# Performance work log

Measured on AMD Instinct MI355X. Metric: run time of the kernel, lower is better.

The kernel has to match this reference:

```python
import jax, jax.numpy as jnp
import numpy as np

B, S, HID = 4, 2048, 1024
H, DH = 16, 64  # HID = H * DH
ADP, NTASKS = 64, 10
GATE_S = 100.0  # s (soft gate temperature), != smax=400 so no hard threshold


def setup_inputs() -> dict:
    key = jax.random.key(0)
    ks = jax.random.split(key, 13)
    sc = 0.02
    return {
        "hidden_states": jax.random.normal(ks[0], (B, S, HID), jnp.float32),
        "Wq": jax.random.normal(ks[1], (HID, HID), jnp.float32) * sc,
        "bq": jax.random.normal(ks[2], (HID,), jnp.float32) * sc,
        "Wk": jax.random.normal(ks[3], (HID, HID), jnp.float32) * sc,
        "bk": jax.random.normal(ks[4], (HID,), jnp.float32) * sc,
        "Wv": jax.random.normal(ks[5], (HID, HID), jnp.float32) * sc,
        "bv": jax.random.normal(ks[6], (HID,), jnp.float32) * sc,
        "fc1_w": jax.random.normal(ks[7], (HID, ADP), jnp.float32) * sc,
        "fc1_b": jax.random.normal(ks[8], (ADP,), jnp.float32) * sc,
        "fc2_w": jax.random.normal(ks[9], (ADP, HID), jnp.float32) * sc,
        "fc2_b": jax.random.normal(ks[10], (HID,), jnp.float32) * sc,
        "efc1": jax.random.normal(ks[11], (NTASKS, ADP), jnp.float32),
        "efc2": jax.random.normal(ks[12], (NTASKS, HID), jnp.float32),
        "t": 3,
    }


def reference(hidden_states, Wq, bq, Wk, bk, Wv, bv,
              fc1_w, fc1_b, fc2_w, fc2_b, efc1, efc2, t):
    x = hidden_states
    # --- parallel adapter with task gates (add_residual=False) ---
    gfc1 = jax.nn.sigmoid(GATE_S * efc1[t])  # [ADP]
    gfc2 = jax.nn.sigmoid(GATE_S * efc2[t])  # [HID]
    h = jax.nn.relu(x @ fc1_w + fc1_b) * gfc1          # [B,S,ADP]
    adapter_out = jax.nn.relu(h @ fc2_w + fc2_b) * gfc2  # [B,S,HID]
    # --- multi-head self-attention (absolute positions, no mask, eval dropout) ---
    def split_heads(y):  # [B,S,HID] -> [B,H,S,DH]
        return y.reshape(B, S, H, DH).transpose(0, 2, 1, 3)
    q = split_heads(x @ Wq + bq)
    k = split_heads(x @ Wk + bk)
    v = split_heads(x @ Wv + bv)
    scores = jnp.einsum("bhqd,bhkd->bhqk", q, k) / np.sqrt(DH).astype(jnp.float32)
    probs = jax.nn.softmax(scores, axis=-1)
    ctx = jnp.einsum("bhqk,bhkd->bhqd", probs, v)
    ctx = ctx.transpose(0, 2, 1, 3).reshape(B, S, HID)
    return ctx + adapter_out
```

## Files before the change

kernel.cpp:

```cpp
#include <hip/hip_runtime.h>
#include <stdint.h>
#include <stddef.h>

typedef unsigned short u16;
typedef unsigned int u32;
typedef __bf16 bf16x8 __attribute__((ext_vector_type(8)));
typedef __bf16 bf16x4 __attribute__((ext_vector_type(4)));
typedef short s16x4 __attribute__((ext_vector_type(4)));
typedef float f32x4 __attribute__((ext_vector_type(4)));

#define BB  4
#define SS  2048
#define HIDD 1024
#define NH  16
#define DHD 64

#define GLD16(gaddr, laddr) \
  __builtin_amdgcn_global_load_lds( \
      (const __attribute__((address_space(1))) u32*)(gaddr), \
      (__attribute__((address_space(3))) u32*)(laddr), 16, 0, 0)

#define LDS_BARRIER() asm volatile("s_waitcnt lgkmcnt(0)\n\ts_barrier" ::: "memory")

#define VMB(n) asm volatile("s_waitcnt vmcnt(" #n ")\n\ts_barrier" ::: "memory")

#if __has_builtin(__builtin_amdgcn_exp2f)
  #define EXP2(x) __builtin_amdgcn_exp2f(x)
#else
  #define EXP2(x) __expf((x) * 0.6931471805599453f)
#endif

__device__ __forceinline__ u16 f2b(float f){
  union { float f; unsigned u; } c; c.f = f;
  unsigned r = c.u + 0x7fffu + ((c.u >> 16) & 1u);
  return (u16)(r >> 16);
}
__device__ __forceinline__ f32x4 mfma32(bf16x8 a, bf16x8 b, f32x4 c){
  return __builtin_amdgcn_mfma_f32_16x16x32_bf16(a, b, c, 0, 0, 0);
}
__device__ __forceinline__ f32x4 mfma16(s16x4 a, s16x4 b, f32x4 c){
  return __builtin_amdgcn_mfma_f32_16x16x16bf16_1k(a, b, c, 0, 0, 0);
}

__global__ __launch_bounds__(256)
void prep(const float* __restrict__ x, u16* __restrict__ xb,
          const float* __restrict__ Wq, const float* __restrict__ Wk,
          const float* __restrict__ Wv, const float* __restrict__ f1w,
          const float* __restrict__ f2w,
          u16* __restrict__ wqkv, u16* __restrict__ wtf1, u16* __restrict__ wtf2)
{
  __shared__ float tile[32][33];
  int blk = blockIdx.x;
  const int tid = threadIdx.x;
  if (blk < 8192) {
    int i = blk * 1024 + tid * 4;
    float4 v = *reinterpret_cast<const float4*>(&x[i]);
    ushort4 o;
    o.x = f2b(v.x); o.y = f2b(v.y); o.z = f2b(v.z); o.w = f2b(v.w);
    *reinterpret_cast<ushort4*>(&xb[i]) = o;
    return;
  }
  blk -= 8192;
  if (blk >= 3200) {
    u16* pad = wqkv + (size_t)3136 * 1024;
    uint4 z = make_uint4(0u, 0u, 0u, 0u);
    *reinterpret_cast<uint4*>(&pad[(size_t)(blk - 3200) * 2048 + tid * 8]) = z;
    return;
  }
  const float* in; u16* out; int R, C, c0, r0;
  if (blk < 3072) {
    int m = blk >> 10, t = blk & 1023;
    in = (m == 0) ? Wq : (m == 1) ? Wk : Wv;
    out = wqkv + (size_t)m * 1024 * 1024;
    R = 1024; C = 1024; c0 = (t & 31) * 32; r0 = (t >> 5) * 32;
  } else if (blk < 3136) {
    int t = blk - 3072;
    in = f1w; out = wtf1; R = 1024; C = 64;
    c0 = (t & 1) * 32; r0 = (t >> 1) * 32;
  } else {
    int t = blk - 3136;
    in = f2w; out = wtf2; R = 64; C = 1024;
    c0 = (t & 31) * 32; r0 = (t >> 5) * 32;
  }
  int tx = tid & 31, ty = tid >> 5;
  #pragma unroll
  for (int j = 0; j < 32; j += 8)
    tile[ty + j][tx] = in[(size_t)(r0 + ty + j) * C + c0 + tx];
  __syncthreads();
  #pragma unroll
  for (int j = 0; j < 32; j += 8)
    out[(size_t)(c0 + ty + j) * R + r0 + tx] = f2b(tile[tx][ty + j]);
}

__global__ __launch_bounds__(256, 2)
void gemm_qkv(const u16* __restrict__ X, const u16* __restrict__ Wt,
              const float* __restrict__ bq, const float* __restrict__ bk,
              const float* __restrict__ bv,
              const float* __restrict__ f1b, const float* __restrict__ efc1,
              const int* __restrict__ tptr,
              u16* __restrict__ qb, u16* __restrict__ kb, u16* __restrict__ vt,
              u16* __restrict__ hb)
{
  constexpr int K = 1024;
  __shared__ __align__(16) u16 ldsA[3][128 * 32];
  __shared__ __align__(16) u16 ldsB[3][256 * 32];
  const int tid = threadIdx.x;
  const int w = tid >> 6, lane = tid & 63, quad = lane >> 4, ln = lane & 15;
  const int id = blockIdx.x;
  const int swz = (id & 7) * 104 + (id >> 3);
  const int m0 = (swz / 13) * 128;
  const int n0 = (swz % 13) * 256;
  const int wrow = (w >> 1) * 64;
  const int wcol = (w & 1) * 128;

  const u16* Xs = X  + (size_t)(m0 + w * 32 + (lane >> 2)) * K + (lane & 3) * 8;
  const u16* Ws = Wt + (size_t)(n0 + w * 64 + (lane >> 2)) * K + (lane & 3) * 8;

  #define STAGE(buf, kk) do { \
    GLD16(Xs + (size_t)(kk),            &ldsA[buf][w * 1024]); \
    GLD16(Xs + (size_t)16 * K + (kk),   &ldsA[buf][w * 1024 + 512]); \
    GLD16(Ws + (size_t)(kk),            &ldsB[buf][w * 2048]); \
    GLD16(Ws + (size_t)16 * K + (kk),   &ldsB[buf][w * 2048 + 512]); \
    GLD16(Ws + (size_t)32 * K + (kk),   &ldsB[buf][w * 2048 + 1024]); \
    GLD16(Ws + (size_t)48 * K + (kk),   &ldsB[buf][w * 2048 + 1536]); \
  } while (0)

  f32x4 acc[4][8] = {};

  STAGE(0, 0);
  STAGE(1, 32);
  VMB(6);

  int cur = 0;
  for (int t = 0; t < 32; ++t) {
    if (t + 2 < 32) {
      int sb = cur + 2; if (sb >= 3) sb -= 3;
      STAGE(sb, (t + 2) * 32);
    }

    bf16x8 a[4], b[8];
    #pragma unroll
    for (int mt = 0; mt < 4; ++mt)
      a[mt] = *reinterpret_cast<const bf16x8*>(
          &ldsA[cur][(wrow + mt * 16 + ln) * 32 + quad * 8]);
    #pragma unroll
    for (int nt = 0; nt < 8; ++nt)
      b[nt] = *reinterpret_cast<const bf16x8*>(
          &ldsB[cur][(wcol + nt * 16 + ln) * 32 + quad * 8]);
    #pragma unroll
    for (int mt = 0; mt < 4; ++mt)
      #pragma unroll
      for (int nt = 0; nt < 8; ++nt)
        acc[mt][nt] = mfma32(a[mt], b[nt], acc[mt][nt]);

    if (t + 2 < 32)      VMB(6);
    else if (t == 30)    VMB(0);

    cur = (cur + 1 == 3) ? 0 : cur + 1;
  }
  #undef STAGE

  if (n0 < 2048) {
    const float scale = (n0 < 1024) ? 0.18033688f : 1.f;
    const float* bias = (n0 < 1024) ? bq : bk;
    u16* dst = (n0 < 1024) ? qb : kb;
    const int nb = n0 & 1023;
    #pragma unroll
    for (int nt = 0; nt < 8; ++nt) {
      const int col = nb + wcol + nt * 16 + ln;
      const float bvv = bias[col];
      #pragma unroll
      for (int mt = 0; mt < 4; ++mt)
        #pragma unroll
        for (int r = 0; r < 4; ++r) {
          int row = m0 + wrow + mt * 16 + quad * 4 + r;
          dst[(size_t)row * 1024 + col] = f2b((acc[mt][nt][r] + bvv) * scale);
        }
    }
  } else if (n0 < 3072) {
    #pragma unroll
    for (int nt = 0; nt < 8; ++nt) {
      const int colv = (n0 - 2048) + wcol + nt * 16 + ln;
      const float bvv = bv[colv];
      const int h = colv >> 6, d2 = colv & 63;
      #pragma unroll
      for (int mt = 0; mt < 4; ++mt) {
        int row = m0 + wrow + mt * 16 + quad * 4;
        int bb = row >> 11, s = row & 2047;
        ushort4 o;
        o.x = f2b(acc[mt][nt][0] + bvv);
        o.y = f2b(acc[mt][nt][1] + bvv);
        o.z = f2b(acc[mt][nt][2] + bvv);
        o.w = f2b(acc[mt][nt][3] + bvv);
        *reinterpret_cast<ushort4*>(
            &vt[((((size_t)bb * NH + h) * DHD + d2) << 11) + s]) = o;
      }
    }
  } else if ((w & 1) == 0) {
    int t = tptr[0];
    if ((unsigned)t > 9u) t = 0;
    #pragma unroll
    for (int nt = 0; nt < 4; ++nt) {
      const int col = nt * 16 + ln;
      const float bvv = f1b[col];
      const float g = 1.f / (1.f + __expf(-100.f * efc1[t * 64 + col]));
      #pragma unroll
      for (int mt = 0; mt < 4; ++mt)
        #pragma unroll
        for (int r = 0; r < 4; ++r) {
          int row = m0 + wrow + mt * 16 + quad * 4 + r;
          hb[(size_t)row * 64 + col] = f2b(fmaxf(acc[mt][nt][r] + bvv, 0.f) * g);
        }
    }
  }
}

__global__ __launch_bounds__(256, 4)
void attn(const u16* __restrict__ Q, const u16* __restrict__ Kb,
          const u16* __restrict__ Vt, const u16* __restrict__ hb,
          const u16* __restrict__ w2, const float* __restrict__ b2,
          const float* __restrict__ gate2, const int* __restrict__ tptr,
          float* __restrict__ out)
{
  __shared__ __align__(16) u16 ldsK[64 * 72];
  __shared__ __align__(16) u16 ldsV[64 * 76];

  const int tid = threadIdx.x;
  const int w = tid >> 6, lane = tid & 63, quad = lane >> 4, ln = lane & 15;
  const int h = blockIdx.x, b = blockIdx.y, qt = blockIdx.z;
  const int bh = b * NH + h;
  const int qbase = qt * 128 + w * 32;
  const int skey = tid >> 3;
  const int sd   = (tid & 7) * 8;

  bf16x8 qf[2][2];
  #pragma unroll
  for (int q2 = 0; q2 < 2; ++q2)
    #pragma unroll
    for (int kk = 0; kk < 2; ++kk)
      qf[q2][kk] = *reinterpret_cast<const bf16x8*>(
          &Q[(size_t)(b * SS + qbase + q2 * 16 + ln) * HIDD + h * DHD + kk * 32 + quad * 8]);

  f32x4 o[4][2] = {};
  f32x4 lacc[2] = {};
  const s16x4 ones = {0x3F80, 0x3F80, 0x3F80, 0x3F80};

  const u16* Kp = &Kb[(size_t)(b * SS + skey) * HIDD + h * DHD + sd];
  const u16* Vp = &Vt[((size_t)bh * DHD + skey) * SS + sd];

  uint4 rK0 = *reinterpret_cast<const uint4*>(Kp);
  uint4 rK1 = *reinterpret_cast<const uint4*>(Kp + (size_t)32 * HIDD);
  uint4 rV0 = *reinterpret_cast<const uint4*>(Vp);
  uint4 rV1 = *reinterpret_cast<const uint4*>(Vp + (size_t)32 * SS);

  for (int kt = 0; kt < SS; kt += 64) {
    LDS_BARRIER();
    *reinterpret_cast<uint4*>(&ldsK[skey * 72 + sd])        = rK0;
    *reinterpret_cast<uint4*>(&ldsK[(32 + skey) * 72 + sd]) = rK1;
    *reinterpret_cast<uint4*>(&ldsV[skey * 76 + sd])        = rV0;
    *reinterpret_cast<uint4*>(&ldsV[(32 + skey) * 76 + sd]) = rV1;
    if (kt + 64 < SS) {
      const u16* Kn = Kp + (size_t)(kt + 64) * HIDD;
      const u16* Vn = Vp + (kt + 64);
      rK0 = *reinterpret_cast<const uint4*>(Kn);
      rK1 = *reinterpret_cast<const uint4*>(Kn + (size_t)32 * HIDD);
      rV0 = *reinterpret_cast<const uint4*>(Vn);
      rV1 = *reinterpret_cast<const uint4*>(Vn + (size_t)32 * SS);
    }
    LDS_BARRIER();

    f32x4 s[4][2];
    __builtin_amdgcn_s_setprio(1);
    #pragma unroll
    for (int k4 = 0; k4 < 4; ++k4) {
      bf16x8 kf0 = *reinterpret_cast<const bf16x8*>(&ldsK[(k4 * 16 + ln) * 72 + quad * 8]);
      bf16x8 kf1 = *reinterpret_cast<const bf16x8*>(&ldsK[(k4 * 16 + ln) * 72 + 32 + quad * 8]);
      #pragma unroll
      for (int q2 = 0; q2 < 2; ++q2) {
        f32x4 z = {0.f, 0.f, 0.f, 0.f};
        z = mfma32(kf0, qf[q2][0], z);
        z = mfma32(kf1, qf[q2][1], z);
        s[k4][q2] = z;
      }
    }
    __builtin_amdgcn_s_setprio(0);

    s16x4 p[4][2];
    #pragma unroll
    for (int k4 = 0; k4 < 4; ++k4)
      #pragma unroll
      for (int q2 = 0; q2 < 2; ++q2) {
        union { bf16x4 b; s16x4 s; } cv;
        #pragma unroll
        for (int r = 0; r < 4; ++r)
          cv.b[r] = (__bf16)EXP2(s[k4][q2][r]);
        p[k4][q2] = cv.s;
      }

    __builtin_amdgcn_s_setprio(1);
    #pragma unroll
    for (int dt = 0; dt < 4; ++dt) {
      #pragma unroll
      for (int ks = 0; ks < 4; ++ks) {
        s16x4 vf = *reinterpret_cast<const s16x4*>(
            &ldsV[(dt * 16 + ln) * 76 + ks * 16 + quad * 4]);
        #pragma unroll
        for (int q2 = 0; q2 < 2; ++q2)
          o[dt][q2] = mfma16(vf, p[ks][q2], o[dt][q2]);
      }
    }
    #pragma unroll
    for (int ks = 0; ks < 4; ++ks)
      #pragma unroll
      for (int q2 = 0; q2 < 2; ++q2)
        lacc[q2] = mfma16(ones, p[ks][q2], lacc[q2]);
    __builtin_amdgcn_s_setprio(0);
  }

  float rl[2];
  #pragma unroll
  for (int q2 = 0; q2 < 2; ++q2)
    rl[q2] = 1.f / lacc[q2][0];

  f32x4 acc2[4][2] = {};
  #pragma unroll
  for (int kk = 0; kk < 2; ++kk) {
    bf16x8 hf[2];
    #pragma unroll
    for (int q2 = 0; q2 < 2; ++q2) {
      int q = qbase + q2 * 16 + ln;
      hf[q2] = *reinterpret_cast<const bf16x8*>(
          &hb[(size_t)(b * SS + q) * 64 + kk * 32 + quad * 8]);
    }
    #pragma unroll
    for (int dt = 0; dt < 4; ++dt) {
      bf16x8 wf = *reinterpret_cast<const bf16x8*>(
          &w2[(size_t)(h * DHD + dt * 16 + ln) * 64 + kk * 32 + quad * 8]);
      #pragma unroll
      for (int q2 = 0; q2 < 2; ++q2)
        acc2[dt][q2] = mfma32(wf, hf[q2], acc2[dt][q2]);
    }
  }

  int t = tptr[0];
  if ((unsigned)t > 9u) t = 0;
  float bv2[4][4], gv2[4][4];
  #pragma unroll
  for (int dt = 0; dt < 4; ++dt)
    #pragma unroll
    for (int r = 0; r < 4; ++r) {
      int col = h * DHD + dt * 16 + quad * 4 + r;
      bv2[dt][r] = b2[col];
      gv2[dt][r] = 1.f / (1.f + __expf(-100.f * gate2[t * HIDD + col]));
    }

  #pragma unroll
  for (int q2 = 0; q2 < 2; ++q2) {
    const int q = qbase + q2 * 16 + ln;
    float* orow = &out[(size_t)(b * SS + q) * HIDD + h * DHD];
    #pragma unroll
    for (int dt = 0; dt < 4; ++dt)
      #pragma unroll
      for (int r = 0; r < 4; ++r) {
        int d = dt * 16 + quad * 4 + r;
        float ad = fmaxf(acc2[dt][q2][r] + bv2[dt][r], 0.f) * gv2[dt][r];
        orow[d] = o[dt][q2][r] * rl[q2] + ad;
      }
  }
}

extern "C" void kernel_launch(void* const* d_in, const int* in_sizes, int n_in,
                              void* d_out, int out_size, void* d_ws, size_t ws_size,
                              hipStream_t stream) {
  const float* x    = (const float*)d_in[0];
  const float* Wq   = (const float*)d_in[1];
  const float* bq   = (const float*)d_in[2];
  const float* Wk   = (const float*)d_in[3];
  const float* bk   = (const float*)d_in[4];
  const float* Wv   = (const float*)d_in[5];
  const float* bv   = (const float*)d_in[6];
  const float* f1w  = (const float*)d_in[7];
  const float* f1b  = (const float*)d_in[8];
  const float* f2w  = (const float*)d_in[9];
  const float* f2b_ = (const float*)d_in[10];
  const float* efc1 = (const float*)d_in[11];
  const float* efc2 = (const float*)d_in[12];
  const int*   tptr = (const int*)d_in[13];
  float* out = (float*)d_out;

  unsigned char* ws = (unsigned char*)d_ws;
  u16* xb   = (u16*)(ws + 0);
  u16* wqkv = (u16*)(ws + (16u << 20));
  u16* wtf1 = wqkv + (size_t)3072 * 1024;
  u16* wtf2 = (u16*)(ws + (22u << 20) + (512u << 10));
  u16* hb   = (u16*)(ws + (23u << 20));
  u16* qb   = (u16*)(ws + (24u << 20));
  u16* kb   = (u16*)(ws + (40u << 20));
  u16* vt   = (u16*)(ws + (56u << 20));

  prep<<<dim3(11488), 256, 0, stream>>>(x, xb, Wq, Wk, Wv, f1w, f2w,
                                        wqkv, wtf1, wtf2);

  gemm_qkv<<<dim3(832), 256, 0, stream>>>(xb, wqkv, bq, bk, bv,
                                          f1b, efc1, tptr, qb, kb, vt, hb);

  attn<<<dim3(NH, BB, SS / 128), 256, 0, stream>>>(
      qb, kb, vt, hb, wtf2, f2b_, efc2, tptr, out);
}
```

Before: 276.4 us.

## Software-pipeline attention: overlap QK^T of next tile with exp and PV of current

Double-buffers the K and V LDS tiles and restructures the key loop so the QK^T MFMAs for tile t+1 are issued alongside the exp2 conversion and PV MFMAs for tile t. A prologue computes the first score tile and an epilogue finishes the last PV step, with the loop manually unrolled by two so the score register sets alternate. The aim is to hide transcendental/VALU latency behind matrix-core work. In exchange LDS usage doubles and register pressure rises from the extra live score tile, which may hurt occupancy at the four-blocks-per-SM launch bound.

```diff
diff --git a/kernel.cpp b/kernel.cpp
--- a/kernel.cpp
+++ b/kernel.cpp
@@ -222,8 +222,8 @@
           const float* __restrict__ gate2, const int* __restrict__ tptr,
           float* __restrict__ out)
 {
-  __shared__ __align__(16) u16 ldsK[64 * 72];
-  __shared__ __align__(16) u16 ldsV[64 * 76];
+  __shared__ __align__(16) u16 ldsK[2][64 * 72];
+  __shared__ __align__(16) u16 ldsV[2][64 * 76];
 
   const int tid = threadIdx.x;
   const int w = tid >> 6, lane = tid & 63, quad = lane >> 4, ln = lane & 15;
@@ -252,39 +252,96 @@
   uint4 rK1 = *reinterpret_cast<const uint4*>(Kp + (size_t)32 * HIDD);
   uint4 rV0 = *reinterpret_cast<const uint4*>(Vp);
   uint4 rV1 = *reinterpret_cast<const uint4*>(Vp + (size_t)32 * SS);
-
-  for (int kt = 0; kt < SS; kt += 64) {
-    LDS_BARRIER();
-    *reinterpret_cast<uint4*>(&ldsK[skey * 72 + sd])        = rK0;
-    *reinterpret_cast<uint4*>(&ldsK[(32 + skey) * 72 + sd]) = rK1;
-    *reinterpret_cast<uint4*>(&ldsV[skey * 76 + sd])        = rV0;
-    *reinterpret_cast<uint4*>(&ldsV[(32 + skey) * 76 + sd]) = rV1;
-    if (kt + 64 < SS) {
-      const u16* Kn = Kp + (size_t)(kt + 64) * HIDD;
-      const u16* Vn = Vp + (kt + 64);
-      rK0 = *reinterpret_cast<const uint4*>(Kn);
-      rK1 = *reinterpret_cast<const uint4*>(Kn + (size_t)32 * HIDD);
-      rV0 = *reinterpret_cast<const uint4*>(Vn);
-      rV1 = *reinterpret_cast<const uint4*>(Vn + (size_t)32 * SS);
-    }
-    LDS_BARRIER();
-
-    f32x4 s[4][2];
-    __builtin_amdgcn_s_setprio(1);
-    #pragma unroll
-    for (int k4 = 0; k4 < 4; ++k4) {
-      bf16x8 kf0 = *reinterpret_cast<const bf16x8*>(&ldsK[(k4 * 16 + ln) * 72 + quad * 8]);
-      bf16x8 kf1 = *reinterpret_cast<const bf16x8*>(&ldsK[(k4 * 16 + ln) * 72 + 32 + quad * 8]);
-      #pragma unroll
-      for (int q2 = 0; q2 < 2; ++q2) {
-        f32x4 z = {0.f, 0.f, 0.f, 0.f};
-        z = mfma32(kf0, qf[q2][0], z);
-        z = mfma32(kf1, qf[q2][1], z);
-        s[k4][q2] = z;
-      }
-    }
-    __builtin_amdgcn_s_setprio(0);
-
+  *reinterpret_cast<uint4*>(&ldsK[0][skey * 72 + sd])        = rK0;
+  *reinterpret_cast<uint4*>(&ldsK[0][(32 + skey) * 72 + sd]) = rK1;
+  *reinterpret_cast<uint4*>(&ldsV[0][skey * 76 + sd])        = rV0;
+  *reinterpret_cast<uint4*>(&ldsV[0][(32 + skey) * 76 + sd]) = rV1;
+  {
+    const u16* Kn = Kp + (size_t)64 * HIDD;
+    const u16* Vn = Vp + 64;
+    rK0 = *reinterpret_cast<const uint4*>(Kn);
+    rK1 = *reinterpret_cast<const uint4*>(Kn + (size_t)32 * HIDD);
+    rV0 = *reinterpret_cast<const uint4*>(Vn);
+    rV1 = *reinterpret_cast<const uint4*>(Vn + (size_t)32 * SS);
+  }
+  LDS_BARRIER();
+
+  f32x4 sA[4][2], sB[4][2];
+  #pragma unroll
+  for (int k4 = 0; k4 < 4; ++k4) {
+    bf16x8 kf0 = *reinterpret_cast<const bf16x8*>(&ldsK[0][(k4 * 16 + ln) * 72 + quad * 8]);
+    bf16x8 kf1 = *reinterpret_cast<const bf16x8*>(&ldsK[0][(k4 * 16 + ln) * 72 + 32 + quad * 8]);
+    #pragma unroll
+    for (int q2 = 0; q2 < 2; ++q2) {
+      f32x4 z = {0.f, 0.f, 0.f, 0.f};
+      z = mfma32(kf0, qf[q2][0], z);
+      z = mfma32(kf1, qf[q2][1], z);
+      sA[k4][q2] = z;
+    }
+  }
+
+  #define STEP(T_, WB_, QB_, VB_, SNEW_, SOLD_, DOLOAD_) do { \
+    LDS_BARRIER(); \
+    *reinterpret_cast<uint4*>(&ldsK[WB_][skey * 72 + sd])        = rK0; \
+    *reinterpret_cast<uint4*>(&ldsK[WB_][(32 + skey) * 72 + sd]) = rK1; \
+    *reinterpret_cast<uint4*>(&ldsV[WB_][skey * 76 + sd])        = rV0; \
+    *reinterpret_cast<uint4*>(&ldsV[WB_][(32 + skey) * 76 + sd]) = rV1; \
+    if (DOLOAD_) { \
+      const u16* Kn = Kp + (size_t)((T_) + 2) * 64 * HIDD; \
+      const u16* Vn = Vp + ((T_) + 2) * 64; \
+      rK0 = *reinterpret_cast<const uint4*>(Kn); \
+      rK1 = *reinterpret_cast<const uint4*>(Kn + (size_t)32 * HIDD); \
+      rV0 = *reinterpret_cast<const uint4*>(Vn); \
+      rV1 = *reinterpret_cast<const uint4*>(Vn + (size_t)32 * SS); \
+    } \
+    LDS_BARRIER(); \
+    s16x4 p[4][2]; \
+    __builtin_amdgcn_s_setprio(1); \
+    _Pragma("unroll") \
+    for (int k4 = 0; k4 < 4; ++k4) { \
+      bf16x8 kf0 = *reinterpret_cast<const bf16x8*>(&ldsK[QB_][(k4 * 16 + ln) * 72 + quad * 8]); \
+      bf16x8 kf1 = *reinterpret_cast<const bf16x8*>(&ldsK[QB_][(k4 * 16 + ln) * 72 + 32 + quad * 8]); \
+      _Pragma("unroll") \
+      for (int q2 = 0; q2 < 2; ++q2) { \
+        f32x4 z = {0.f, 0.f, 0.f, 0.f}; \
+        z = mfma32(kf0, qf[q2][0], z); \
+        z = mfma32(kf1, qf[q2][1], z); \
+        SNEW_[k4][q2] = z; \
+      } \
+      _Pragma("unroll") \
+      for (int q2 = 0; q2 < 2; ++q2) { \
+        union { bf16x4 b; s16x4 s; } cv; \
+        _Pragma("unroll") \
+        for (int r = 0; r < 4; ++r) \
+          cv.b[r] = (__bf16)EXP2(SOLD_[k4][q2][r]); \
+        p[k4][q2] = cv.s; \
+      } \
+    } \
+    _Pragma("unroll") \
+    for (int dt = 0; dt < 4; ++dt) \
+      _Pragma("unroll") \
+      for (int ks = 0; ks < 4; ++ks) { \
+        s16x4 vf = *reinterpret_cast<const s16x4*>( \
+            &ldsV[VB_][(dt * 16 + ln) * 76 + ks * 16 + quad * 4]); \
+        _Pragma("unroll") \
+        for (int q2 = 0; q2 < 2; ++q2) \
+          o[dt][q2] = mfma16(vf, p[ks][q2], o[dt][q2]); \
+      } \
+    _Pragma("unroll") \
+    for (int ks = 0; ks < 4; ++ks) \
+      _Pragma("unroll") \
+      for (int q2 = 0; q2 < 2; ++q2) \
+        lacc[q2] = mfma16(ones, p[ks][q2], lacc[q2]); \
+    __builtin_amdgcn_s_setprio(0); \
+  } while (0)
+
+  for (int tt = 0; tt < 30; tt += 2) {
+    STEP(tt,     1, 1, 0, sB, sA, 1);
+    STEP(tt + 1, 0, 0, 1, sA, sB, 1);
+  }
+  STEP(30, 1, 1, 0, sB, sA, 0);
+  #undef STEP
+  {
     s16x4 p[4][2];
     #pragma unroll
     for (int k4 = 0; k4 < 4; ++k4)
@@ -293,22 +350,20 @@
         union { bf16x4 b; s16x4 s; } cv;
         #pragma unroll
         for (int r = 0; r < 4; ++r)
-          cv.b[r] = (__bf16)EXP2(s[k4][q2][r]);
+          cv.b[r] = (__bf16)EXP2(sB[k4][q2][r]);
         p[k4][q2] = cv.s;
       }
-
     __builtin_amdgcn_s_setprio(1);
     #pragma unroll
-    for (int dt = 0; dt < 4; ++dt) {
+    for (int dt = 0; dt < 4; ++dt)
       #pragma unroll
       for (int ks = 0; ks < 4; ++ks) {
         s16x4 vf = *reinterpret_cast<const s16x4*>(
-            &ldsV[(dt * 16 + ln) * 76 + ks * 16 + quad * 4]);
+            &ldsV[1][(dt * 16 + ln) * 76 + ks * 16 + quad * 4]);
         #pragma unroll
         for (int q2 = 0; q2 < 2; ++q2)
           o[dt][q2] = mfma16(vf, p[ks][q2], o[dt][q2]);
       }
-    }
     #pragma unroll
     for (int ks = 0; ks < 4; ++ks)
       #pragma unroll
```

Result: slower. 608.6 us (+120.1%).
